# Performance work log

Hardware: AMD Instinct MI355X
Metric: run time of the kernel (lower is better)

The kernel has to match this reference:

```python
import jax, jax.numpy as jnp
import numpy as np
from jax import lax

EPS = 1e-5


def _conv1d(x, w, groups=1):
    # x: [B, Cin, L], w: [Cout, Cin/groups, K], padding=1, stride=1
    return lax.conv_general_dilated(
        x, w, window_strides=(1,), padding=[(1, 1)],
        dimension_numbers=('NCH', 'OIH', 'NCH'),
        feature_group_count=groups)


def _batchnorm(x, gamma, beta):
    # training-mode BatchNorm1d: stats over (batch, length), biased variance
    mean = jnp.mean(x, axis=(0, 2), keepdims=True)
    var = jnp.mean(jnp.square(x - mean), axis=(0, 2), keepdims=True)
    xn = (x - mean) * lax.rsqrt(var + EPS)
    return xn * gamma[None, :, None] + beta[None, :, None]


def setup_inputs() -> dict:
    key = jax.random.key(0)
    ks = jax.random.split(key, 8)
    B = 1 << 20  # 1,048,576
    x = jax.random.normal(ks[0], (B, 3), dtype=jnp.float32)
    # conv1: 1 -> 16, k=3 (xavier-normal-ish scale)
    w1 = jax.random.normal(ks[1], (16, 1, 3), dtype=jnp.float32) * 0.5
    b1 = jnp.zeros((16,), jnp.float32)
    g1 = jnp.ones((16,), jnp.float32)
    bt1 = jnp.zeros((16,), jnp.float32)
    # conv2: grouped, groups=16, 16 -> 32, k=3 -> weight [32, 1, 3]
    w2 = jax.random.normal(ks[2], (32, 1, 3), dtype=jnp.float32) * 0.5
    b2 = jnp.zeros((32,), jnp.float32)
    g2 = jnp.ones((32,), jnp.float32)
    bt2 = jnp.zeros((32,), jnp.float32)
    # fc1: Linear(32 -> 16) kaiming-normal-ish
    fw1 = jax.random.normal(ks[3], (16, 32), dtype=jnp.float32) * (2.0 / 32.0) ** 0.5
    fb1 = jnp.zeros((16,), jnp.float32)
    # fc2: Linear(16 -> 1); torch init sets these to 0, but use small random
    # values so gradients/outputs are non-degenerate for testing
    fw2 = jax.random.normal(ks[4], (1, 16), dtype=jnp.float32) * 0.1
    fb2 = jnp.zeros((1,), jnp.float32)
    return dict(x=x, w1=w1, b1=b1, g1=g1, bt1=bt1,
                w2=w2, b2=b2, g2=g2, bt2=bt2,
                fw1=fw1, fb1=fb1, fw2=fw2, fb2=fb2)


def reference(x, w1, b1, g1, bt1, w2, b2, g2, bt2, fw1, fb1, fw2, fb2):
    h = x[:, None, :]                                   # [B, 1, 3]
    h = _conv1d(h, w1) + b1[None, :, None]              # [B, 16, 3]
    h = _batchnorm(jax.nn.relu(h), g1, bt1)
    h = _conv1d(h, w2, groups=16) + b2[None, :, None]   # [B, 32, 3]
    h = _batchnorm(jax.nn.relu(h), g2, bt2)
    h = jnp.mean(h, axis=2)                             # AdaptiveAvgPool1d(1) -> [B, 32]
    h = jax.nn.relu(h @ fw1.T + fb1)                    # [B, 16]
    return h @ fw2.T + fb2                              # [B, 1]
```

## Files before the change

### kernel.cpp

```cpp
#include <hip/hip_runtime.h>
#include <math.h>

#define EPSV 1e-5f

__device__ __forceinline__ void conv3_relu(float x0, float x1, float x2,
                                           float wa, float wb, float wc, float bb,
                                           float& t0, float& t1, float& t2)
{
    t0 = fmaxf(fmaf(wb, x0, fmaf(wc, x1, bb)), 0.f);
    t1 = fmaxf(fmaf(wa, x0, fmaf(wb, x1, fmaf(wc, x2, bb))), 0.f);
    t2 = fmaxf(fmaf(wa, x1, fmaf(wb, x2, bb)), 0.f);
}

__global__ __launch_bounds__(256) void k_stats1(const float* __restrict__ x,
                                                const float* __restrict__ w1,
                                                const float* __restrict__ b1,
                                                float* __restrict__ partials,
                                                int B)
{
    __shared__ float4 sW1[16];
    int t = threadIdx.x;
    if (t < 16) sW1[t] = make_float4(w1[3*t], w1[3*t+1], w1[3*t+2], b1[t]);
    __syncthreads();

    float cur[32];
#pragma unroll
    for (int i = 0; i < 32; ++i) cur[i] = 0.f;

    auto upd = [&](int g, float t0, float t1, float t2) {
        cur[g]      += t0 + t1 + t2;
        cur[16 + g]  = fmaf(t0, t0, fmaf(t1, t1, fmaf(t2, t2, cur[16 + g])));
    };

    auto accum1 = [&](float x0, float x1, float x2) {
#pragma unroll
        for (int g = 0; g < 16; ++g) {
            float4 w = sW1[g];
            float t0, t1, t2;
            conv3_relu(x0, x1, x2, w.x, w.y, w.z, w.w, t0, t1, t2);
            upd(g, t0, t1, t2);
        }
    };

    int nchunk = (B + 3) >> 2;
    for (int ch = blockIdx.x * 256 + t; ch < nchunk; ch += gridDim.x * 256) {
        int s0 = ch << 2;
        if (s0 + 4 <= B) {
            const float4* xp = (const float4*)(x + (size_t)s0 * 3);
            float4 A = xp[0], Bq = xp[1], Cq = xp[2];
            const float xs[4][3] = {{A.x,  A.y,  A.z },
                                    {A.w,  Bq.x, Bq.y},
                                    {Bq.z, Bq.w, Cq.x},
                                    {Cq.y, Cq.z, Cq.w}};
#pragma unroll
            for (int g = 0; g < 16; ++g) {
                float4 w = sW1[g];
#pragma unroll
                for (int m = 0; m < 4; ++m) {
                    float t0, t1, t2;
                    conv3_relu(xs[m][0], xs[m][1], xs[m][2],
                               w.x, w.y, w.z, w.w, t0, t1, t2);
                    upd(g, t0, t1, t2);
                }
            }
        } else {
            for (int m = 0; m < 4; ++m) {
                int s = s0 + m;
                if (s < B) accum1(x[3*s], x[3*s+1], x[3*s+2]);
            }
        }
    }

    int lane = t & 63, wid = t >> 6;
#pragma unroll
    for (int i = 0; i < 32; ++i) cur[i] += __shfl_xor(cur[i], 32, 64);
#pragma unroll
    for (int half = 16; half >= 1; half >>= 1) {
#pragma unroll
        for (int i = 0; i < half; ++i) {
            bool up = (lane & half);
            float keep = up ? cur[i + half] : cur[i];
            float send = up ? cur[i] : cur[i + half];
            cur[i] = keep + __shfl_xor(send, half, 64);
        }
    }
    __shared__ float red[4][32];
    if (lane < 32) red[wid][lane] = cur[0];
    __syncthreads();
    if (t < 32)
        partials[blockIdx.x * 32 + t] = red[0][t] + red[1][t] + red[2][t] + red[3][t];
}

__global__ __launch_bounds__(256) void k_fin1(const float* __restrict__ partials,
                                              const float* __restrict__ g1,
                                              const float* __restrict__ bt1,
                                              const float* __restrict__ w2,
                                              const float* __restrict__ b2,
                                              float* __restrict__ w2f,
                                              float* __restrict__ b2f,
                                              float Ninv, int nb)
{
    __shared__ float4 red4[32][8];
    __shared__ float tot[32];
    __shared__ float ssc[16], ssh[16];
    int t = threadIdx.x;
    {
        int v4 = t & 7, c = t >> 3;
        float4 a = make_float4(0.f, 0.f, 0.f, 0.f);
        for (int b = c; b < nb; b += 32) {
            float4 p = ((const float4*)partials)[b * 8 + v4];
            a.x += p.x; a.y += p.y; a.z += p.z; a.w += p.w;
        }
        red4[c][v4] = a;
    }
    __syncthreads();
    if (t < 8) {
        float4 a = make_float4(0.f, 0.f, 0.f, 0.f);
#pragma unroll
        for (int c = 0; c < 32; ++c) {
            float4 p = red4[c][t];
            a.x += p.x; a.y += p.y; a.z += p.z; a.w += p.w;
        }
        tot[4*t+0] = a.x; tot[4*t+1] = a.y; tot[4*t+2] = a.z; tot[4*t+3] = a.w;
    }
    __syncthreads();
    if (t < 16) {
        float mean = tot[t] * Ninv;
        float var  = fmaxf(tot[16 + t] * Ninv - mean * mean, 0.f);
        float rstd = rsqrtf(var + EPSV);
        float sc = g1[t] * rstd;
        ssc[t] = sc;
        ssh[t] = bt1[t] - mean * sc;
    }
    __syncthreads();
    if (t < 96) {
        int o = t / 3, p = t % 3;
        int g = o >> 1;
        w2f[t] = w2[t] * ssc[g];
        float wv0 = w2[3*o], wv1 = w2[3*o+1], wv2 = w2[3*o+2];
        float sv = (p == 0) ? (wv1 + wv2) : ((p == 1) ? (wv0 + wv1 + wv2) : (wv0 + wv1));
        b2f[t] = b2[o] + ssh[g] * sv;
    }
}

__global__ __launch_bounds__(256) void k_stats2(const float* __restrict__ x,
                                                const float* __restrict__ w1,
                                                const float* __restrict__ b1,
                                                const float* __restrict__ w2f,
                                                const float* __restrict__ b2f,
                                                float* __restrict__ partials,
                                                int B)
{
    __shared__ float4 sW1[16];
    __shared__ float4 sU[32];
    __shared__ float2 sC[32];
    int t = threadIdx.x;
    if (t < 16) sW1[t] = make_float4(w1[3*t], w1[3*t+1], w1[3*t+2], b1[t]);
    else if (t >= 32 && t < 64) {
        int o = t - 32;
        sU[o] = make_float4(w2f[3*o], w2f[3*o+1], w2f[3*o+2], b2f[3*o]);
        sC[o] = make_float2(b2f[3*o+1], b2f[3*o+2]);
    }
    __syncthreads();

    const int p = t & 1;
    const int gbase = 8 * p;

    float cur[32];
#pragma unroll
    for (int i = 0; i < 32; ++i) cur[i] = 0.f;

    auto updc = [&](int oc, float v0, float v1, float v2) {
        cur[oc]      += v0 + v1 + v2;
        cur[16 + oc]  = fmaf(v0, v0, fmaf(v1, v1, fmaf(v2, v2, cur[16 + oc])));
    };

    auto accum4 = [&](const float4& A, const float4& Bq, const float4& Cq) {
        const float xs[4][3] = {{A.x,  A.y,  A.z },
                                {A.w,  Bq.x, Bq.y},
                                {Bq.z, Bq.w, Cq.x},
                                {Cq.y, Cq.z, Cq.w}};
#pragma unroll
        for (int g = 0; g < 8; ++g) {
            float4 w = sW1[gbase + g];
            float r[4][3];
#pragma unroll
            for (int m = 0; m < 4; ++m)
                conv3_relu(xs[m][0], xs[m][1], xs[m][2],
                           w.x, w.y, w.z, w.w, r[m][0], r[m][1], r[m][2]);
#pragma unroll
            for (int jj = 0; jj < 2; ++jj) {
                int oc = 2 * g + jj;
                int oo = 16 * p + oc;
                float4 u = sU[oo];
                float2 cc = sC[oo];
#pragma unroll
                for (int m = 0; m < 4; ++m) {
                    float v0 = fmaxf(fmaf(u.y, r[m][0], fmaf(u.z, r[m][1], u.w)), 0.f);
                    float v1 = fmaxf(fmaf(u.x, r[m][0], fmaf(u.y, r[m][1], fmaf(u.z, r[m][2], cc.x))), 0.f);
                    float v2 = fmaxf(fmaf(u.x, r[m][1], fmaf(u.y, r[m][2], cc.y)), 0.f);
                    updc(oc, v0, v1, v2);
                }
            }
        }
    };

    auto accum1 = [&](float x0, float x1, float x2) {
#pragma unroll
        for (int g = 0; g < 8; ++g) {
            float4 w = sW1[gbase + g];
            float r0, r1, r2;
            conv3_relu(x0, x1, x2, w.x, w.y, w.z, w.w, r0, r1, r2);
#pragma unroll
            for (int jj = 0; jj < 2; ++jj) {
                int oc = 2 * g + jj;
                int oo = 16 * p + oc;
                float4 u = sU[oo];
                float2 cc = sC[oo];
                float v0 = fmaxf(fmaf(u.y, r0, fmaf(u.z, r1, u.w)), 0.f);
                float v1 = fmaxf(fmaf(u.x, r0, fmaf(u.y, r1, fmaf(u.z, r2, cc.x))), 0.f);
                float v2 = fmaxf(fmaf(u.x, r1, fmaf(u.y, r2, cc.y)), 0.f);
                updc(oc, v0, v1, v2);
            }
        }
    };

    int nchunk = (B + 3) >> 2;
    int gp     = (blockIdx.x * 256 + t) >> 1;
    int stride = (gridDim.x * 256) >> 1;
    for (int ch = gp; ch < nchunk; ch += stride) {
        int s0 = ch << 2;
        if (s0 + 4 <= B) {
            const float4* xp = (const float4*)(x + (size_t)s0 * 3);
            float4 A = xp[0], Bq = xp[1], Cq = xp[2];
            accum4(A, Bq, Cq);
        } else {
            for (int m = 0; m < 4; ++m) {
                int s = s0 + m;
                if (s < B) accum1(x[3*s], x[3*s+1], x[3*s+2]);
            }
        }
    }

    int lane = t & 63, wid = t >> 6;
#pragma unroll
    for (int half = 16; half >= 1; half >>= 1) {
        int d = half << 1;
#pragma unroll
        for (int i = 0; i < half; ++i) {
            bool up = (lane & d);
            float keep = up ? cur[i + half] : cur[i];
            float send = up ? cur[i] : cur[i + half];
            cur[i] = keep + __shfl_xor(send, d, 64);
        }
    }
    __shared__ float red[4][64];
    {
        int idx = lane >> 1;
        int v = ((idx >> 4) << 5) + 16 * p + (idx & 15);
        red[wid][v] = cur[0];
    }
    __syncthreads();
    if (t < 64)
        partials[blockIdx.x * 64 + t] = red[0][t] + red[1][t] + red[2][t] + red[3][t];
}

__global__ __launch_bounds__(256) void k_fin2(const float* __restrict__ partials,
                                              const float* __restrict__ g2,
                                              const float* __restrict__ bt2,
                                              const float* __restrict__ fw1,
                                              const float* __restrict__ fb1,
                                              float* __restrict__ fw1sT,
                                              float* __restrict__ c1,
                                              float Ninv, int nb)
{
    __shared__ float4 red4[16][16];
    __shared__ float tot[64];
    __shared__ float ssc[32], ssh[32];
    int t = threadIdx.x;
    {
        int v4 = t & 15, c = t >> 4;
        float4 a = make_float4(0.f, 0.f, 0.f, 0.f);
        for (int b = c; b < nb; b += 16) {
            float4 p = ((const float4*)partials)[b * 16 + v4];
            a.x += p.x; a.y += p.y; a.z += p.z; a.w += p.w;
        }
        red4[c][v4] = a;
    }
    __syncthreads();
    if (t < 16) {
        float4 a = make_float4(0.f, 0.f, 0.f, 0.f);
#pragma unroll
        for (int c = 0; c < 16; ++c) {
            float4 p = red4[c][t];
            a.x += p.x; a.y += p.y; a.z += p.z; a.w += p.w;
        }
        tot[4*t+0] = a.x; tot[4*t+1] = a.y; tot[4*t+2] = a.z; tot[4*t+3] = a.w;
    }
    __syncthreads();
    if (t < 32) {
        float mean = tot[t] * Ninv;
        float var  = fmaxf(tot[32 + t] * Ninv - mean * mean, 0.f);
        float rstd = rsqrtf(var + EPSV);
        float sc = g2[t] * rstd;
        ssc[t] = sc;
        ssh[t] = bt2[t] - mean * sc;
    }
    __syncthreads();
    for (int idx = t; idx < 512; idx += 256) {
        int o = idx >> 4, j = idx & 15;
        fw1sT[idx] = fw1[j * 32 + o] * ssc[o] * (1.0f / 3.0f);
    }
    if (t < 16) {
        float a = fb1[t];
#pragma unroll
        for (int c = 0; c < 32; ++c) a = fmaf(fw1[t * 32 + c], ssh[c], a);
        c1[t] = a;
    }
}

__global__ __launch_bounds__(256) void k_final(const float* __restrict__ x,
                                               const float* __restrict__ w1,
                                               const float* __restrict__ b1,
                                               const float* __restrict__ w2f,
                                               const float* __restrict__ b2f,
                                               const float* __restrict__ fw1sT,
                                               const float* __restrict__ c1,
                                               const float* __restrict__ fw2,
                                               const float* __restrict__ fb2,
                                               float* __restrict__ out,
                                               int B)
{
    __shared__ float4 sW1[16];
    __shared__ float4 sU[32];
    __shared__ float2 sC[32];
    __shared__ float4 sFT[128];
    __shared__ float2 sJ[16];
    __shared__ float  sb2;
    int t = threadIdx.x;
    if (t < 16) sW1[t] = make_float4(w1[3*t], w1[3*t+1], w1[3*t+2], b1[t]);
    else if (t >= 32 && t < 64) {
        int o = t - 32;
        sU[o] = make_float4(w2f[3*o], w2f[3*o+1], w2f[3*o+2], b2f[3*o]);
        sC[o] = make_float2(b2f[3*o+1], b2f[3*o+2]);
    } else if (t >= 64 && t < 192) {
        sFT[t - 64] = ((const float4*)fw1sT)[t - 64];
    } else if (t >= 192 && t < 208) {
        sJ[t - 192] = make_float2(c1[t - 192], fw2[t - 192]);
    } else if (t == 224) {
        sb2 = fb2[0];
    }
    __syncthreads();

    int nchunk = (B + 3) >> 2;
    for (int ch = blockIdx.x * 256 + t; ch < nchunk; ch += gridDim.x * 256) {
        int s0 = ch << 2;
        if (s0 + 4 <= B) {
            const float4* xp = (const float4*)(x + (size_t)s0 * 3);
            float4 A = xp[0], Bq = xp[1], Cq = xp[2];
            const float xs[4][3] = {{A.x,  A.y,  A.z },
                                    {A.w,  Bq.x, Bq.y},
                                    {Bq.z, Bq.w, Cq.x},
                                    {Cq.y, Cq.z, Cq.w}};

            float acc[4][16];
#pragma unroll
            for (int m = 0; m < 4; ++m)
#pragma unroll
                for (int j = 0; j < 16; ++j) acc[m][j] = 0.f;

#pragma unroll 4
            for (int g = 0; g < 16; ++g) {
                float4 w = sW1[g];
                float r[4][3];
#pragma unroll
                for (int m = 0; m < 4; ++m)
                    conv3_relu(xs[m][0], xs[m][1], xs[m][2],
                               w.x, w.y, w.z, w.w, r[m][0], r[m][1], r[m][2]);
#pragma unroll
                for (int jj = 0; jj < 2; ++jj) {
                    int o = 2 * g + jj;
                    float4 u = sU[o];
                    float2 cc = sC[o];
                    float so[4];
#pragma unroll
                    for (int m = 0; m < 4; ++m) {
                        float v0 = fmaxf(fmaf(u.y, r[m][0], fmaf(u.z, r[m][1], u.w)), 0.f);
                        float v1 = fmaxf(fmaf(u.x, r[m][0], fmaf(u.y, r[m][1], fmaf(u.z, r[m][2], cc.x))), 0.f);
                        float v2 = fmaxf(fmaf(u.x, r[m][1], fmaf(u.y, r[m][2], cc.y)), 0.f);
                        so[m] = v0 + v1 + v2;
                    }
#pragma unroll
                    for (int k = 0; k < 4; ++k) {
                        float4 f = sFT[o * 4 + k];
#pragma unroll
                        for (int m = 0; m < 4; ++m) {
                            acc[m][4*k+0] = fmaf(f.x, so[m], acc[m][4*k+0]);
                            acc[m][4*k+1] = fmaf(f.y, so[m], acc[m][4*k+1]);
                            acc[m][4*k+2] = fmaf(f.z, so[m], acc[m][4*k+2]);
                            acc[m][4*k+3] = fmaf(f.w, so[m], acc[m][4*k+3]);
                        }
                    }
                }
            }

            float res[4];
#pragma unroll
            for (int m = 0; m < 4; ++m) res[m] = sb2;
#pragma unroll
            for (int j = 0; j < 16; ++j) {
                float2 jw = sJ[j];
#pragma unroll
                for (int m = 0; m < 4; ++m)
                    res[m] = fmaf(jw.y, fmaxf(acc[m][j] + jw.x, 0.f), res[m]);
            }
            *(float4*)(out + s0) = make_float4(res[0], res[1], res[2], res[3]);
        } else {
            for (int m = 0; m < 4; ++m) {
                int s = s0 + m;
                if (s >= B) break;
                float x0 = x[3*s], x1 = x[3*s+1], x2 = x[3*s+2];
                float acc1[16];
#pragma unroll
                for (int j = 0; j < 16; ++j) acc1[j] = 0.f;
#pragma unroll 4
                for (int g = 0; g < 16; ++g) {
                    float4 w = sW1[g];
                    float r0, r1, r2;
                    conv3_relu(x0, x1, x2, w.x, w.y, w.z, w.w, r0, r1, r2);
#pragma unroll
                    for (int jj = 0; jj < 2; ++jj) {
                        int o = 2 * g + jj;
                        float4 u = sU[o];
                        float2 cc = sC[o];
                        float v0 = fmaxf(fmaf(u.y, r0, fmaf(u.z, r1, u.w)), 0.f);
                        float v1 = fmaxf(fmaf(u.x, r0, fmaf(u.y, r1, fmaf(u.z, r2, cc.x))), 0.f);
                        float v2 = fmaxf(fmaf(u.x, r1, fmaf(u.y, r2, cc.y)), 0.f);
                        float so = v0 + v1 + v2;
#pragma unroll
                        for (int k = 0; k < 4; ++k) {
                            float4 f = sFT[o * 4 + k];
                            acc1[4*k+0] = fmaf(f.x, so, acc1[4*k+0]);
                            acc1[4*k+1] = fmaf(f.y, so, acc1[4*k+1]);
                            acc1[4*k+2] = fmaf(f.z, so, acc1[4*k+2]);
                            acc1[4*k+3] = fmaf(f.w, so, acc1[4*k+3]);
                        }
                    }
                }
                float r = sb2;
#pragma unroll
                for (int j = 0; j < 16; ++j) {
                    float2 jw = sJ[j];
                    r = fmaf(jw.y, fmaxf(acc1[j] + jw.x, 0.f), r);
                }
                out[s] = r;
            }
        }
    }
}

extern "C" void kernel_launch(void* const* d_in, const int* in_sizes, int n_in,
                              void* d_out, int out_size, void* d_ws, size_t ws_size,
                              hipStream_t stream)
{
    const float* x   = (const float*)d_in[0];
    const float* w1  = (const float*)d_in[1];
    const float* b1  = (const float*)d_in[2];
    const float* g1  = (const float*)d_in[3];
    const float* bt1 = (const float*)d_in[4];
    const float* w2  = (const float*)d_in[5];
    const float* b2  = (const float*)d_in[6];
    const float* g2  = (const float*)d_in[7];
    const float* bt2 = (const float*)d_in[8];
    const float* fw1 = (const float*)d_in[9];
    const float* fb1 = (const float*)d_in[10];
    const float* fw2 = (const float*)d_in[11];
    const float* fb2 = (const float*)d_in[12];

    int B = in_sizes[0] / 3;

    int nb1 = 512;
    int nb2 = 1024;
    while ((size_t)(nb1 * 32 + nb2 * 64 + 720) * sizeof(float) > ws_size && nb1 > 1) {
        nb1 >>= 1; nb2 >>= 1;
    }

    float* ws    = (float*)d_ws;
    float* p1    = ws;
    float* p2    = ws + (size_t)nb1 * 32;
    float* w2f   = p2 + (size_t)nb2 * 64;
    float* b2f   = w2f + 96;
    float* fw1sT = b2f + 96;
    float* c1    = fw1sT + 512;

    float Ninv = 1.0f / (3.0f * (float)B);

    int nchunk = (B + 3) / 4;
    int gridF = (nchunk + 255) / 256;
    if (gridF > 2048) gridF = 2048;

    k_stats1<<<nb1, 256, 0, stream>>>(x, w1, b1, p1, B);
    k_fin1<<<1, 256, 0, stream>>>(p1, g1, bt1, w2, b2, w2f, b2f, Ninv, nb1);
    k_stats2<<<nb2, 256, 0, stream>>>(x, w1, b1, w2f, b2f, p2, B);
    k_fin2<<<1, 256, 0, stream>>>(p2, g2, bt2, fw1, fb1, fw1sT, c1, Ninv, nb2);
    k_final<<<gridF, 256, 0, stream>>>(x, w1, b1, w2f, b2f, fw1sT, c1,
                                       fw2, fb2, (float*)d_out, B);
}
```

Before: 171.9 us.

## Fold single-block BN finalize kernels into the consuming kernels

Removes the two single-block finalize kernels: each block of the second-stats kernel and of the final kernel now reduces the stage partials itself and computes the folded BN scales and weights in shared memory. This cuts two kernel launches and their serial single-block latency, in exchange for every block redundantly re-reading the partial arrays. The second-stats grid shrinks from 1024 to 512 blocks to keep that redundant reduction small, and the main loop unroll drops from 4 to 2, likely to contain register pressure.

```diff
diff --git a/kernel.cpp b/kernel.cpp
--- a/kernel.cpp
+++ b/kernel.cpp
@@ -91,34 +91,41 @@
         partials[blockIdx.x * 32 + t] = red[0][t] + red[1][t] + red[2][t] + red[3][t];
 }
 
-__global__ __launch_bounds__(256) void k_fin1(const float* __restrict__ partials,
-                                              const float* __restrict__ g1,
-                                              const float* __restrict__ bt1,
-                                              const float* __restrict__ w2,
-                                              const float* __restrict__ b2,
-                                              float* __restrict__ w2f,
-                                              float* __restrict__ b2f,
-                                              float Ninv, int nb)
+__global__ __launch_bounds__(256) void k_stats2(const float* __restrict__ x,
+                                                const float* __restrict__ w1,
+                                                const float* __restrict__ b1,
+                                                const float* __restrict__ p1,
+                                                const float* __restrict__ g1,
+                                                const float* __restrict__ bt1,
+                                                const float* __restrict__ w2,
+                                                const float* __restrict__ b2,
+                                                float* __restrict__ partials,
+                                                float Ninv, int nb1, int B)
 {
-    __shared__ float4 red4[32][8];
+    __shared__ float4 sW1[16];
+    __shared__ float4 sU[32];
+    __shared__ float2 sC[32];
+    __shared__ float4 redbuf[256];
     __shared__ float tot[32];
     __shared__ float ssc[16], ssh[16];
     int t = threadIdx.x;
+
     {
         int v4 = t & 7, c = t >> 3;
         float4 a = make_float4(0.f, 0.f, 0.f, 0.f);
-        for (int b = c; b < nb; b += 32) {
-            float4 p = ((const float4*)partials)[b * 8 + v4];
+        for (int b = c; b < nb1; b += 32) {
+            float4 p = ((const float4*)p1)[b * 8 + v4];
             a.x += p.x; a.y += p.y; a.z += p.z; a.w += p.w;
         }
-        red4[c][v4] = a;
-    }
+        redbuf[c * 8 + v4] = a;
+    }
+    if (t < 16) sW1[t] = make_float4(w1[3*t], w1[3*t+1], w1[3*t+2], b1[t]);
     __syncthreads();
     if (t < 8) {
         float4 a = make_float4(0.f, 0.f, 0.f, 0.f);
 #pragma unroll
         for (int c = 0; c < 32; ++c) {
-            float4 p = red4[c][t];
+            float4 p = redbuf[c * 8 + t];
             a.x += p.x; a.y += p.y; a.z += p.z; a.w += p.w;
         }
         tot[4*t+0] = a.x; tot[4*t+1] = a.y; tot[4*t+2] = a.z; tot[4*t+3] = a.w;
@@ -133,33 +140,14 @@
         ssh[t] = bt1[t] - mean * sc;
     }
     __syncthreads();
-    if (t < 96) {
-        int o = t / 3, p = t % 3;
-        int g = o >> 1;
-        w2f[t] = w2[t] * ssc[g];
+    if (t < 32) {
+        int o = t, g = o >> 1;
+        float sc = ssc[g], sh = ssh[g];
         float wv0 = w2[3*o], wv1 = w2[3*o+1], wv2 = w2[3*o+2];
-        float sv = (p == 0) ? (wv1 + wv2) : ((p == 1) ? (wv0 + wv1 + wv2) : (wv0 + wv1));
-        b2f[t] = b2[o] + ssh[g] * sv;
-    }
-}
-
-__global__ __launch_bounds__(256) void k_stats2(const float* __restrict__ x,
-                                                const float* __restrict__ w1,
-                                                const float* __restrict__ b1,
-                                                const float* __restrict__ w2f,
-                                                const float* __restrict__ b2f,
-                                                float* __restrict__ partials,
-                                                int B)
-{
-    __shared__ float4 sW1[16];
-    __shared__ float4 sU[32];
-    __shared__ float2 sC[32];
-    int t = threadIdx.x;
-    if (t < 16) sW1[t] = make_float4(w1[3*t], w1[3*t+1], w1[3*t+2], b1[t]);
-    else if (t >= 32 && t < 64) {
-        int o = t - 32;
-        sU[o] = make_float4(w2f[3*o], w2f[3*o+1], w2f[3*o+2], b2f[3*o]);
-        sC[o] = make_float2(b2f[3*o+1], b2f[3*o+2]);
+        sU[o] = make_float4(wv0 * sc, wv1 * sc, wv2 * sc,
+                            b2[o] + sh * (wv1 + wv2));
+        sC[o] = make_float2(b2[o] + sh * (wv0 + wv1 + wv2),
+                            b2[o] + sh * (wv0 + wv1));
     }
     __syncthreads();
 
@@ -265,71 +253,23 @@
         partials[blockIdx.x * 64 + t] = red[0][t] + red[1][t] + red[2][t] + red[3][t];
 }
 
-__global__ __launch_bounds__(256) void k_fin2(const float* __restrict__ partials,
-                                              const float* __restrict__ g2,
-                                              const float* __restrict__ bt2,
-                                              const float* __restrict__ fw1,
-                                              const float* __restrict__ fb1,
-                                              float* __restrict__ fw1sT,
-                                              float* __restrict__ c1,
-                                              float Ninv, int nb)
-{
-    __shared__ float4 red4[16][16];
-    __shared__ float tot[64];
-    __shared__ float ssc[32], ssh[32];
-    int t = threadIdx.x;
-    {
-        int v4 = t & 15, c = t >> 4;
-        float4 a = make_float4(0.f, 0.f, 0.f, 0.f);
-        for (int b = c; b < nb; b += 16) {
-            float4 p = ((const float4*)partials)[b * 16 + v4];
-            a.x += p.x; a.y += p.y; a.z += p.z; a.w += p.w;
-        }
-        red4[c][v4] = a;
-    }
-    __syncthreads();
-    if (t < 16) {
-        float4 a = make_float4(0.f, 0.f, 0.f, 0.f);
-#pragma unroll
-        for (int c = 0; c < 16; ++c) {
-            float4 p = red4[c][t];
-            a.x += p.x; a.y += p.y; a.z += p.z; a.w += p.w;
-        }
-        tot[4*t+0] = a.x; tot[4*t+1] = a.y; tot[4*t+2] = a.z; tot[4*t+3] = a.w;
-    }
-    __syncthreads();
-    if (t < 32) {
-        float mean = tot[t] * Ninv;
-        float var  = fmaxf(tot[32 + t] * Ninv - mean * mean, 0.f);
-        float rstd = rsqrtf(var + EPSV);
-        float sc = g2[t] * rstd;
-        ssc[t] = sc;
-        ssh[t] = bt2[t] - mean * sc;
-    }
-    __syncthreads();
-    for (int idx = t; idx < 512; idx += 256) {
-        int o = idx >> 4, j = idx & 15;
-        fw1sT[idx] = fw1[j * 32 + o] * ssc[o] * (1.0f / 3.0f);
-    }
-    if (t < 16) {
-        float a = fb1[t];
-#pragma unroll
-        for (int c = 0; c < 32; ++c) a = fmaf(fw1[t * 32 + c], ssh[c], a);
-        c1[t] = a;
-    }
-}
-
 __global__ __launch_bounds__(256) void k_final(const float* __restrict__ x,
                                                const float* __restrict__ w1,
                                                const float* __restrict__ b1,
-                                               const float* __restrict__ w2f,
-                                               const float* __restrict__ b2f,
-                                               const float* __restrict__ fw1sT,
-                                               const float* __restrict__ c1,
+                                               const float* __restrict__ w2,
+                                               const float* __restrict__ b2,
+                                               const float* __restrict__ g1,
+                                               const float* __restrict__ bt1,
+                                               const float* __restrict__ g2,
+                                               const float* __restrict__ bt2,
+                                               const float* __restrict__ fw1,
+                                               const float* __restrict__ fb1,
                                                const float* __restrict__ fw2,
                                                const float* __restrict__ fb2,
+                                               const float* __restrict__ p1,
+                                               const float* __restrict__ p2,
                                                float* __restrict__ out,
-                                               int B)
+                                               float Ninv, int nb1, int nb2, int B)
 {
     __shared__ float4 sW1[16];
     __shared__ float4 sU[32];
@@ -337,18 +277,91 @@
     __shared__ float4 sFT[128];
     __shared__ float2 sJ[16];
     __shared__ float  sb2;
+    __shared__ float4 redbuf[256];
+    __shared__ float tot1[32];
+    __shared__ float tot2[64];
+    __shared__ float ssc1[16], ssh1[16];
+    __shared__ float ssc2[32], ssh2[32];
     int t = threadIdx.x;
+
+    {
+        int v4 = t & 7, c = t >> 3;
+        float4 a = make_float4(0.f, 0.f, 0.f, 0.f);
+        for (int b = c; b < nb1; b += 32) {
+            float4 p = ((const float4*)p1)[b * 8 + v4];
+            a.x += p.x; a.y += p.y; a.z += p.z; a.w += p.w;
+        }
+        redbuf[c * 8 + v4] = a;
+    }
     if (t < 16) sW1[t] = make_float4(w1[3*t], w1[3*t+1], w1[3*t+2], b1[t]);
-    else if (t >= 32 && t < 64) {
-        int o = t - 32;
-        sU[o] = make_float4(w2f[3*o], w2f[3*o+1], w2f[3*o+2], b2f[3*o]);
-        sC[o] = make_float2(b2f[3*o+1], b2f[3*o+2]);
-    } else if (t >= 64 && t < 192) {
-        sFT[t - 64] = ((const float4*)fw1sT)[t - 64];
-    } else if (t >= 192 && t < 208) {
-        sJ[t - 192] = make_float2(c1[t - 192], fw2[t - 192]);
-    } else if (t == 224) {
-        sb2 = fb2[0];
+    if (t == 224) sb2 = fb2[0];
+    __syncthreads();
+    if (t < 8) {
+        float4 a = make_float4(0.f, 0.f, 0.f, 0.f);
+#pragma unroll
+        for (int c = 0; c < 32; ++c) {
+            float4 p = redbuf[c * 8 + t];
+            a.x += p.x; a.y += p.y; a.z += p.z; a.w += p.w;
+        }
+        tot1[4*t+0] = a.x; tot1[4*t+1] = a.y; tot1[4*t+2] = a.z; tot1[4*t+3] = a.w;
+    }
+    __syncthreads();
+    if (t < 16) {
+        float mean = tot1[t] * Ninv;
+        float var  = fmaxf(tot1[16 + t] * Ninv - mean * mean, 0.f);
+        float rstd = rsqrtf(var + EPSV);
+        float sc = g1[t] * rstd;
+        ssc1[t] = sc;
+        ssh1[t] = bt1[t] - mean * sc;
+    }
+    __syncthreads();
+    if (t < 32) {
+        int o = t, g = o >> 1;
+        float sc = ssc1[g], sh = ssh1[g];
+        float wv0 = w2[3*o], wv1 = w2[3*o+1], wv2 = w2[3*o+2];
+        sU[o] = make_float4(wv0 * sc, wv1 * sc, wv2 * sc,
+                            b2[o] + sh * (wv1 + wv2));
+        sC[o] = make_float2(b2[o] + sh * (wv0 + wv1 + wv2),
+                            b2[o] + sh * (wv0 + wv1));
+    }
+    {
+        int v4 = t & 15, c = t >> 4;
+        float4 a = make_float4(0.f, 0.f, 0.f, 0.f);
+        for (int b = c; b < nb2; b += 16) {
+            float4 p = ((const float4*)p2)[b * 16 + v4];
+            a.x += p.x; a.y += p.y; a.z += p.z; a.w += p.w;
+        }
+        redbuf[c * 16 + v4] = a;
+    }
+    __syncthreads();
+    if (t < 16) {
+        float4 a = make_float4(0.f, 0.f, 0.f, 0.f);
+#pragma unroll
+        for (int c = 0; c < 16; ++c) {
+            float4 p = redbuf[c * 16 + t];
+            a.x += p.x; a.y += p.y; a.z += p.z; a.w += p.w;
+        }
+        tot2[4*t+0] = a.x; tot2[4*t+1] = a.y; tot2[4*t+2] = a.z; tot2[4*t+3] = a.w;
+    }
+    __syncthreads();
+    if (t < 32) {
+        float mean = tot2[t] * Ninv;
+        float var  = fmaxf(tot2[32 + t] * Ninv - mean * mean, 0.f);
+        float rstd = rsqrtf(var + EPSV);
+        float sc = g2[t] * rstd;
+        ssc2[t] = sc;
+        ssh2[t] = bt2[t] - mean * sc;
+    }
+    __syncthreads();
+    for (int idx = t; idx < 512; idx += 256) {
+        int o = idx >> 4, j = idx & 15;
+        ((float*)sFT)[o * 16 + j] = fw1[j * 32 + o] * ssc2[o] * (1.0f / 3.0f);
+    }
+    if (t < 16) {
+        float a = fb1[t];
+#pragma unroll
+        for (int c = 0; c < 32; ++c) a = fmaf(fw1[t * 32 + c], ssh2[c], a);
+        sJ[t] = make_float2(a, fw2[t]);
     }
     __syncthreads();
 
@@ -369,7 +382,7 @@
 #pragma unroll
                 for (int j = 0; j < 16; ++j) acc[m][j] = 0.f;
 
-#pragma unroll 4
+#pragma unroll 2
             for (int g = 0; g < 16; ++g) {
                 float4 w = sW1[g];
                 float r[4][3];
@@ -423,7 +436,7 @@
                 float acc1[16];
 #pragma unroll
                 for (int j = 0; j < 16; ++j) acc1[j] = 0.f;
-#pragma unroll 4
+#pragma unroll 2
                 for (int g = 0; g < 16; ++g) {
                     float4 w = sW1[g];
                     float r0, r1, r2;
@@ -480,18 +493,14 @@
     int B = in_sizes[0] / 3;
 
     int nb1 = 512;
-    int nb2 = 1024;
-    while ((size_t)(nb1 * 32 + nb2 * 64 + 720) * sizeof(float) > ws_size && nb1 > 1) {
+    int nb2 = 512;
+    while ((size_t)(nb1 * 32 + nb2 * 64) * sizeof(float) > ws_size && nb1 > 1) {
         nb1 >>= 1; nb2 >>= 1;
     }
 
-    float* ws    = (float*)d_ws;
-    float* p1    = ws;
-    float* p2    = ws + (size_t)nb1 * 32;
-    float* w2f   = p2 + (size_t)nb2 * 64;
-    float* b2f   = w2f + 96;
-    float* fw1sT = b2f + 96;
-    float* c1    = fw1sT + 512;
+    float* ws = (float*)d_ws;
+    float* p1 = ws;
+    float* p2 = ws + (size_t)nb1 * 32;
 
     float Ninv = 1.0f / (3.0f * (float)B);
 
@@ -500,9 +509,9 @@
     if (gridF > 2048) gridF = 2048;
 
     k_stats1<<<nb1, 256, 0, stream>>>(x, w1, b1, p1, B);
-    k_fin1<<<1, 256, 0, stream>>>(p1, g1, bt1, w2, b2, w2f, b2f, Ninv, nb1);
-    k_stats2<<<nb2, 256, 0, stream>>>(x, w1, b1, w2f, b2f, p2, B);
-    k_fin2<<<1, 256, 0, stream>>>(p2, g2, bt2, fw1, fb1, fw1sT, c1, Ninv, nb2);
-    k_final<<<gridF, 256, 0, stream>>>(x, w1, b1, w2f, b2f, fw1sT, c1,
-                                       fw2, fb2, (float*)d_out, B);
+    k_stats2<<<nb2, 256, 0, stream>>>(x, w1, b1, p1, g1, bt1, w2, b2,
+                                      p2, Ninv, nb1, B);
+    k_final<<<gridF, 256, 0, stream>>>(x, w1, b1, w2, b2, g1, bt1, g2, bt2,
+                                       fw1, fb1, fw2, fb2, p1, p2,
+                                       (float*)d_out, Ninv, nb1, nb2, B);
 }
```

After: 162.7 us. 1.06x faster.

## Fold BN finalize kernels into stats2 with redundant prologue and last-block epilogue

Applied to the files above, without the earlier changes.

Removes the two single-block finalize kernels. Each k_stats2 block now reduces the stage-1 partials itself to build the folded conv2 weights. The last block to finish, found with an atomic counter and threadfence, computes the stage-2 BN fold and the fc1 prep. The k_stats2 grid also drops from 1024 to 512 blocks. This cuts two launches and their serialization, at the cost of every block re-reading the 512x32 partials and an extra memset for the counter.

```diff
diff --git a/kernel.cpp b/kernel.cpp
--- a/kernel.cpp
+++ b/kernel.cpp
@@ -11,6 +11,7 @@
     t1 = fmaxf(fmaf(wa, x0, fmaf(wb, x1, fmaf(wc, x2, bb))), 0.f);
     t2 = fmaxf(fmaf(wa, x1, fmaf(wb, x2, bb)), 0.f);
 }
+
 
 __global__ __launch_bounds__(256) void k_stats1(const float* __restrict__ x,
                                                 const float* __restrict__ w1,
@@ -91,34 +92,50 @@
         partials[blockIdx.x * 32 + t] = red[0][t] + red[1][t] + red[2][t] + red[3][t];
 }
 
-__global__ __launch_bounds__(256) void k_fin1(const float* __restrict__ partials,
-                                              const float* __restrict__ g1,
-                                              const float* __restrict__ bt1,
-                                              const float* __restrict__ w2,
-                                              const float* __restrict__ b2,
-                                              float* __restrict__ w2f,
-                                              float* __restrict__ b2f,
-                                              float Ninv, int nb)
+__global__ __launch_bounds__(256) void k_stats2(const float* __restrict__ x,
+                                                const float* __restrict__ w1,
+                                                const float* __restrict__ b1,
+                                                const float* __restrict__ p1,
+                                                const float* __restrict__ g1,
+                                                const float* __restrict__ bt1,
+                                                const float* __restrict__ w2,
+                                                const float* __restrict__ b2,
+                                                const float* __restrict__ g2,
+                                                const float* __restrict__ bt2,
+                                                const float* __restrict__ fw1,
+                                                const float* __restrict__ fb1,
+                                                float* __restrict__ partials,
+                                                float4* __restrict__ wU,
+                                                float2* __restrict__ wC,
+                                                float* __restrict__ fw1sT,
+                                                float* __restrict__ c1,
+                                                int* __restrict__ cnt,
+                                                float Ninv, int nb1, int B)
 {
-    __shared__ float4 red4[32][8];
-    __shared__ float tot[32];
-    __shared__ float ssc[16], ssh[16];
+    __shared__ float4 sW1[16];
+    __shared__ float4 sU[32];
+    __shared__ float2 sC[32];
+    __shared__ float4 redbuf[256];
+    __shared__ float tot[64];
+    __shared__ float ssc[32], ssh[32];
     int t = threadIdx.x;
+
     {
         int v4 = t & 7, c = t >> 3;
         float4 a = make_float4(0.f, 0.f, 0.f, 0.f);
-        for (int b = c; b < nb; b += 32) {
-            float4 p = ((const float4*)partials)[b * 8 + v4];
+        for (int b = c; b < nb1; b += 32) {
+            float4 p = ((const float4*)p1)[b * 8 + v4];
             a.x += p.x; a.y += p.y; a.z += p.z; a.w += p.w;
         }
-        red4[c][v4] = a;
-    }
+        redbuf[c * 8 + v4] = a;
+    }
+    if (t < 16) sW1[t] = make_float4(w1[3*t], w1[3*t+1], w1[3*t+2], b1[t]);
     __syncthreads();
     if (t < 8) {
         float4 a = make_float4(0.f, 0.f, 0.f, 0.f);
 #pragma unroll
         for (int c = 0; c < 32; ++c) {
-            float4 p = red4[c][t];
+            float4 p = redbuf[c * 8 + t];
             a.x += p.x; a.y += p.y; a.z += p.z; a.w += p.w;
         }
         tot[4*t+0] = a.x; tot[4*t+1] = a.y; tot[4*t+2] = a.z; tot[4*t+3] = a.w;
@@ -133,35 +150,17 @@
         ssh[t] = bt1[t] - mean * sc;
     }
     __syncthreads();
-    if (t < 96) {
-        int o = t / 3, p = t % 3;
-        int g = o >> 1;
-        w2f[t] = w2[t] * ssc[g];
+    if (t < 32) {
+        int o = t, g = o >> 1;
+        float sc = ssc[g], sh = ssh[g];
         float wv0 = w2[3*o], wv1 = w2[3*o+1], wv2 = w2[3*o+2];
-        float sv = (p == 0) ? (wv1 + wv2) : ((p == 1) ? (wv0 + wv1 + wv2) : (wv0 + wv1));
-        b2f[t] = b2[o] + ssh[g] * sv;
-    }
-}
-
-__global__ __launch_bounds__(256) void k_stats2(const float* __restrict__ x,
-                                                const float* __restrict__ w1,
-                                                const float* __restrict__ b1,
-                                                const float* __restrict__ w2f,
-                                                const float* __restrict__ b2f,
-                                                float* __restrict__ partials,
-                                                int B)
-{
-    __shared__ float4 sW1[16];
-    __shared__ float4 sU[32];
-    __shared__ float2 sC[32];
-    int t = threadIdx.x;
-    if (t < 16) sW1[t] = make_float4(w1[3*t], w1[3*t+1], w1[3*t+2], b1[t]);
-    else if (t >= 32 && t < 64) {
-        int o = t - 32;
-        sU[o] = make_float4(w2f[3*o], w2f[3*o+1], w2f[3*o+2], b2f[3*o]);
-        sC[o] = make_float2(b2f[3*o+1], b2f[3*o+2]);
-    }
-    __syncthreads();
+        sU[o] = make_float4(wv0 * sc, wv1 * sc, wv2 * sc,
+                            b2[o] + sh * (wv1 + wv2));
+        sC[o] = make_float2(b2[o] + sh * (wv0 + wv1 + wv2),
+                            b2[o] + sh * (wv0 + wv1));
+    }
+    __syncthreads();
+    if (blockIdx.x == 0 && t < 32) { wU[t] = sU[t]; wC[t] = sC[t]; }
 
     const int p = t & 1;
     const int gbase = 8 * p;
@@ -263,67 +262,65 @@
     __syncthreads();
     if (t < 64)
         partials[blockIdx.x * 64 + t] = red[0][t] + red[1][t] + red[2][t] + red[3][t];
-}
-
-__global__ __launch_bounds__(256) void k_fin2(const float* __restrict__ partials,
-                                              const float* __restrict__ g2,
-                                              const float* __restrict__ bt2,
-                                              const float* __restrict__ fw1,
-                                              const float* __restrict__ fb1,
-                                              float* __restrict__ fw1sT,
-                                              float* __restrict__ c1,
-                                              float Ninv, int nb)
-{
-    __shared__ float4 red4[16][16];
-    __shared__ float tot[64];
-    __shared__ float ssc[32], ssh[32];
-    int t = threadIdx.x;
-    {
-        int v4 = t & 15, c = t >> 4;
-        float4 a = make_float4(0.f, 0.f, 0.f, 0.f);
-        for (int b = c; b < nb; b += 16) {
-            float4 p = ((const float4*)partials)[b * 16 + v4];
-            a.x += p.x; a.y += p.y; a.z += p.z; a.w += p.w;
-        }
-        red4[c][v4] = a;
-    }
-    __syncthreads();
-    if (t < 16) {
-        float4 a = make_float4(0.f, 0.f, 0.f, 0.f);
-#pragma unroll
-        for (int c = 0; c < 16; ++c) {
-            float4 p = red4[c][t];
-            a.x += p.x; a.y += p.y; a.z += p.z; a.w += p.w;
-        }
-        tot[4*t+0] = a.x; tot[4*t+1] = a.y; tot[4*t+2] = a.z; tot[4*t+3] = a.w;
-    }
-    __syncthreads();
-    if (t < 32) {
-        float mean = tot[t] * Ninv;
-        float var  = fmaxf(tot[32 + t] * Ninv - mean * mean, 0.f);
-        float rstd = rsqrtf(var + EPSV);
-        float sc = g2[t] * rstd;
-        ssc[t] = sc;
-        ssh[t] = bt2[t] - mean * sc;
-    }
-    __syncthreads();
-    for (int idx = t; idx < 512; idx += 256) {
-        int o = idx >> 4, j = idx & 15;
-        fw1sT[idx] = fw1[j * 32 + o] * ssc[o] * (1.0f / 3.0f);
-    }
-    if (t < 16) {
-        float a = fb1[t];
-#pragma unroll
-        for (int c = 0; c < 32; ++c) a = fmaf(fw1[t * 32 + c], ssh[c], a);
-        c1[t] = a;
+
+    __shared__ int isLastS;
+    __threadfence();
+    __syncthreads();
+    if (t == 0) {
+        int prev = atomicAdd(cnt, 1);
+        isLastS = (prev == (int)gridDim.x - 1);
+    }
+    __syncthreads();
+    if (isLastS) {
+        __threadfence();
+        int NBg = gridDim.x;
+        {
+            int v4 = t & 15, c = t >> 4;
+            float4 a = make_float4(0.f, 0.f, 0.f, 0.f);
+            for (int b = c; b < NBg; b += 16) {
+                float4 p = ((const float4*)partials)[b * 16 + v4];
+                a.x += p.x; a.y += p.y; a.z += p.z; a.w += p.w;
+            }
+            redbuf[c * 16 + v4] = a;
+        }
+        __syncthreads();
+        if (t < 16) {
+            float4 a = make_float4(0.f, 0.f, 0.f, 0.f);
+#pragma unroll
+            for (int c = 0; c < 16; ++c) {
+                float4 p = redbuf[c * 16 + t];
+                a.x += p.x; a.y += p.y; a.z += p.z; a.w += p.w;
+            }
+            tot[4*t+0] = a.x; tot[4*t+1] = a.y; tot[4*t+2] = a.z; tot[4*t+3] = a.w;
+        }
+        __syncthreads();
+        if (t < 32) {
+            float mean = tot[t] * Ninv;
+            float var  = fmaxf(tot[32 + t] * Ninv - mean * mean, 0.f);
+            float rstd = rsqrtf(var + EPSV);
+            float sc = g2[t] * rstd;
+            ssc[t] = sc;
+            ssh[t] = bt2[t] - mean * sc;
+        }
+        __syncthreads();
+        for (int idx = t; idx < 512; idx += 256) {
+            int o = idx >> 4, j = idx & 15;
+            fw1sT[idx] = fw1[j * 32 + o] * ssc[o] * (1.0f / 3.0f);
+        }
+        if (t < 16) {
+            float a = fb1[t];
+#pragma unroll
+            for (int c = 0; c < 32; ++c) a = fmaf(fw1[t * 32 + c], ssh[c], a);
+            c1[t] = a;
+        }
     }
 }
 
 __global__ __launch_bounds__(256) void k_final(const float* __restrict__ x,
                                                const float* __restrict__ w1,
                                                const float* __restrict__ b1,
-                                               const float* __restrict__ w2f,
-                                               const float* __restrict__ b2f,
+                                               const float4* __restrict__ wU,
+                                               const float2* __restrict__ wC,
                                                const float* __restrict__ fw1sT,
                                                const float* __restrict__ c1,
                                                const float* __restrict__ fw2,
@@ -341,8 +338,8 @@
     if (t < 16) sW1[t] = make_float4(w1[3*t], w1[3*t+1], w1[3*t+2], b1[t]);
     else if (t >= 32 && t < 64) {
         int o = t - 32;
-        sU[o] = make_float4(w2f[3*o], w2f[3*o+1], w2f[3*o+2], b2f[3*o]);
-        sC[o] = make_float2(b2f[3*o+1], b2f[3*o+2]);
+        sU[o] = wU[o];
+        sC[o] = wC[o];
     } else if (t >= 64 && t < 192) {
         sFT[t - 64] = ((const float4*)fw1sT)[t - 64];
     } else if (t >= 192 && t < 208) {
@@ -480,18 +477,20 @@
     int B = in_sizes[0] / 3;
 
     int nb1 = 512;
-    int nb2 = 1024;
-    while ((size_t)(nb1 * 32 + nb2 * 64 + 720) * sizeof(float) > ws_size && nb1 > 1) {
+    int nb2 = 512;
+    while ((size_t)(nb1 * 32 + nb2 * 64 + 128 + 64 + 512 + 16 + 1) * sizeof(float)
+               > ws_size && nb1 > 1) {
         nb1 >>= 1; nb2 >>= 1;
     }
 
-    float* ws    = (float*)d_ws;
-    float* p1    = ws;
-    float* p2    = ws + (size_t)nb1 * 32;
-    float* w2f   = p2 + (size_t)nb2 * 64;
-    float* b2f   = w2f + 96;
-    float* fw1sT = b2f + 96;
-    float* c1    = fw1sT + 512;
+    float*  ws    = (float*)d_ws;
+    float*  p1    = ws;
+    float*  p2    = ws + (size_t)nb1 * 32;
+    float4* wU    = (float4*)(p2 + (size_t)nb2 * 64);
+    float2* wC    = (float2*)((float*)wU + 128);
+    float*  fw1sT = (float*)wC + 64;
+    float*  c1    = fw1sT + 512;
+    int*    cnt   = (int*)(c1 + 16);
 
     float Ninv = 1.0f / (3.0f * (float)B);
 
@@ -499,10 +498,12 @@
     int gridF = (nchunk + 255) / 256;
     if (gridF > 2048) gridF = 2048;
 
+    hipMemsetAsync(cnt, 0, sizeof(int), stream);
+
     k_stats1<<<nb1, 256, 0, stream>>>(x, w1, b1, p1, B);
-    k_fin1<<<1, 256, 0, stream>>>(p1, g1, bt1, w2, b2, w2f, b2f, Ninv, nb1);
-    k_stats2<<<nb2, 256, 0, stream>>>(x, w1, b1, w2f, b2f, p2, B);
-    k_fin2<<<1, 256, 0, stream>>>(p2, g2, bt2, fw1, fb1, fw1sT, c1, Ninv, nb2);
-    k_final<<<gridF, 256, 0, stream>>>(x, w1, b1, w2f, b2f, fw1sT, c1,
+    k_stats2<<<nb2, 256, 0, stream>>>(x, w1, b1, p1, g1, bt1, w2, b2, g2, bt2,
+                                      fw1, fb1, p2, wU, wC, fw1sT, c1, cnt,
+                                      Ninv, nb1, B);
+    k_final<<<gridF, 256, 0, stream>>>(x, w1, b1, wU, wC, fw1sT, c1,
                                        fw2, fb2, (float*)d_out, B);
 }
```

Result: slower. 191.0 us (+11.1%).
